# Performance work log

Hardware: AMD Instinct MI355X
Metric: run time of the kernel (lower is better)

Reference implementation:

```python
import jax, jax.numpy as jnp
import numpy as np

T, HID, H, KV, D = 2048, 2048, 16, 8, 128
EPS = 1e-6
THETA = 10000.0


def setup_inputs() -> dict:
    key = jax.random.key(0)
    ks = jax.random.split(key, 4)
    return {
        "positions": jnp.arange(T, dtype=jnp.int32),
        "hidden_states": jax.random.normal(ks[0], (T, HID), dtype=jnp.float32),
        "layernorm_weight": jnp.ones((HID,), dtype=jnp.float32),
        "qkv_weight": jax.random.normal(ks[1], ((H + 2 * KV) * D, HID), dtype=jnp.float32) * 0.02,
        "q_norm_weight": jnp.ones((D,), dtype=jnp.float32),
        "k_norm_weight": jnp.ones((D,), dtype=jnp.float32),
        "o_weight": jax.random.normal(ks[2], (HID, H * D), dtype=jnp.float32) * 0.02,
    }


def _rms(x, w, eps=EPS):
    var = jnp.mean(jnp.square(x), axis=-1, keepdims=True)
    return x * jax.lax.rsqrt(var + eps) * w


def _rope(x, pos):
    # NeoX-style rotary over full head_dim. x: [T, nH, D]
    inv_freq = 1.0 / (THETA ** (jnp.arange(0, D, 2, dtype=jnp.float32) / D))
    ang = pos.astype(jnp.float32)[:, None] * inv_freq  # [T, D/2]
    cos, sin = jnp.cos(ang)[:, None, :], jnp.sin(ang)[:, None, :]
    x1, x2 = x[..., : D // 2], x[..., D // 2 :]
    return jnp.concatenate([x1 * cos - x2 * sin, x2 * cos + x1 * sin], axis=-1)


def reference(positions, hidden_states, layernorm_weight, qkv_weight,
              q_norm_weight, k_norm_weight, o_weight):
    # Fused RMSNorm + QKV projection
    normed = _rms(hidden_states, layernorm_weight)                 # [T, HID]
    qkv = normed @ qkv_weight.T                                    # [T, (H+2KV)*D]
    q, k, v = jnp.split(qkv, [H * D, (H + KV) * D], axis=-1)
    q = _rms(q.reshape(T, H, D), q_norm_weight)                    # per-head q norm
    k = _rms(k.reshape(T, KV, D), k_norm_weight)                   # per-head k norm
    v = v.reshape(T, KV, D)
    # RoPE
    q = _rope(q, positions)
    k = _rope(k, positions)
    # GQA causal attention
    scale = D ** -0.5
    kr = jnp.repeat(k, H // KV, axis=1)                            # [T, H, D]
    vr = jnp.repeat(v, H // KV, axis=1)
    scores = jnp.einsum("qhd,khd->hqk", q, kr) * scale             # [H, T, T]
    mask = jnp.tril(jnp.ones((T, T), dtype=bool))
    scores = jnp.where(mask[None], scores, jnp.finfo(scores.dtype).min)
    attn = jax.nn.softmax(scores, axis=-1)
    out = jnp.einsum("hqk,khd->qhd", attn, vr).reshape(T, H * D)
    return out @ o_weight.T                                        # [T, HID]
```

## Files before the change

kernel.cpp:

```cpp
#include <hip/hip_runtime.h>
#include <cstdint>
#include <cstddef>

typedef __bf16 bf16;
typedef __attribute__((ext_vector_type(8))) __bf16 bf16x8;
typedef __attribute__((ext_vector_type(4))) __bf16 bf16x4v;
typedef __attribute__((ext_vector_type(4))) float f32x4;
typedef __attribute__((ext_vector_type(4))) short short4v;

#define T_N   2048
#define HID_N 2048
#define NH    16
#define NKV   8
#define HD    128

#define MFMA(a, b, c) __builtin_amdgcn_mfma_f32_16x16x32_bf16((a), (b), (c), 0, 0, 0)

__device__ __forceinline__ f32x4 MFMA16(short4v a, short4v b, f32x4 c) {
#if __has_builtin(__builtin_amdgcn_mfma_f32_16x16x16bf16_1k)
    return __builtin_amdgcn_mfma_f32_16x16x16bf16_1k(a, b, c, 0, 0, 0);
#else
    asm volatile("v_mfma_f32_16x16x16_bf16 %0, %1, %2, %0\n\ts_nop 7\n\ts_nop 7"
                 : "+v"(c) : "v"(a), "v"(b));
    return c;
#endif
}

__device__ __forceinline__ void gl_lds16(const void* g, void* l) {
    __builtin_amdgcn_global_load_lds(
        (const __attribute__((address_space(1))) unsigned int*)g,
        (__attribute__((address_space(3))) unsigned int*)l,
        16, 0, 0);
}

__device__ __forceinline__ uint32_t pk2(float a, float b) {
    union { bf16 h; unsigned short u; } ca, cb;
    ca.h = (bf16)a; cb.h = (bf16)b;
    return ((uint32_t)cb.u << 16) | ca.u;
}

__global__ __launch_bounds__(256) void k_f2b(const float* __restrict__ in,
                                             bf16* __restrict__ out, int n) {
    int i = (blockIdx.x * 256 + threadIdx.x) * 8;
    if (i >= n) return;
    const float4* p = (const float4*)(in + i);
    float4 a = p[0], b = p[1];
    bf16x8 v;
    v[0] = (bf16)a.x; v[1] = (bf16)a.y; v[2] = (bf16)a.z; v[3] = (bf16)a.w;
    v[4] = (bf16)b.x; v[5] = (bf16)b.y; v[6] = (bf16)b.z; v[7] = (bf16)b.w;
    *(bf16x8*)(out + i) = v;
}

__global__ __launch_bounds__(256) void k_rmsnorm(const float* __restrict__ x,
                                                 const float* __restrict__ w,
                                                 bf16* __restrict__ out) {
    int row = blockIdx.x, tid = threadIdx.x;
    const float* xr = x + (size_t)row * HID_N;
    float4 a = ((const float4*)xr)[tid * 2];
    float4 b = ((const float4*)xr)[tid * 2 + 1];
    float ss = a.x*a.x + a.y*a.y + a.z*a.z + a.w*a.w
             + b.x*b.x + b.y*b.y + b.z*b.z + b.w*b.w;
    #pragma unroll
    for (int m = 32; m; m >>= 1) ss += __shfl_xor(ss, m);
    __shared__ float red[4];
    if ((tid & 63) == 0) red[tid >> 6] = ss;
    __syncthreads();
    float tot = red[0] + red[1] + red[2] + red[3];
    float rs = rsqrtf(tot * (1.0f / HID_N) + 1e-6f);
    const float4* wr = (const float4*)(w + tid * 8);
    float4 wa = wr[0], wb = wr[1];
    bf16x8 v;
    v[0] = (bf16)(a.x * rs * wa.x); v[1] = (bf16)(a.y * rs * wa.y);
    v[2] = (bf16)(a.z * rs * wa.z); v[3] = (bf16)(a.w * rs * wa.w);
    v[4] = (bf16)(b.x * rs * wb.x); v[5] = (bf16)(b.y * rs * wb.y);
    v[6] = (bf16)(b.z * rs * wb.z); v[7] = (bf16)(b.w * rs * wb.w);
    *(bf16x8*)(out + (size_t)row * HID_N + tid * 8) = v;
}

__global__ __launch_bounds__(256, 3) void k_gemm_bt(const bf16* __restrict__ A,
                                                    const bf16* __restrict__ B,
                                                    float* __restrict__ C,
                                                    int M, int N, int K) {
    __shared__ __attribute__((aligned(16))) bf16 As[128 * 64];
    __shared__ __attribute__((aligned(16))) bf16 Bs[128 * 64];
    const int tid = threadIdx.x;
    const int lane = tid & 63, wid = tid >> 6;
    const int wm = wid >> 1, wn = wid & 1;
    const int r = lane & 15, g = lane >> 4;
    const size_t bm = (size_t)blockIdx.y * 128, bn = (size_t)blockIdx.x * 128;

    f32x4 acc[4][4] = {};

    const int srow = tid >> 3;
    const int schk = tid & 7;

    for (int k0 = 0; k0 < K; k0 += 64) {
        __syncthreads();
        #pragma unroll
        for (int c = 0; c < 4; c++) {
            int row = c * 32 + srow;
            int ka = (schk ^ (row & 7)) << 3;
            gl_lds16(A + (bm + row) * (size_t)K + k0 + ka,
                     (char*)As + c * 4096 + tid * 16);
            gl_lds16(B + (bn + row) * (size_t)K + k0 + ka,
                     (char*)Bs + c * 4096 + tid * 16);
        }
        __syncthreads();
        #pragma unroll
        for (int kk = 0; kk < 2; kk++) {
            bf16x8 af[4], bfr[4];
            #pragma unroll
            for (int m = 0; m < 4; m++) {
                int row = wm * 64 + m * 16 + r;
                af[m] = *(const bf16x8*)(As + row * 64 + (((kk * 4 + g) ^ (row & 7)) << 3));
            }
            #pragma unroll
            for (int n = 0; n < 4; n++) {
                int row = wn * 64 + n * 16 + r;
                bfr[n] = *(const bf16x8*)(Bs + row * 64 + (((kk * 4 + g) ^ (row & 7)) << 3));
            }
            #pragma unroll
            for (int m = 0; m < 4; m++)
                #pragma unroll
                for (int n = 0; n < 4; n++)
                    acc[m][n] = MFMA(af[m], bfr[n], acc[m][n]);
        }
    }
    #pragma unroll
    for (int m = 0; m < 4; m++)
        #pragma unroll
        for (int n = 0; n < 4; n++)
            #pragma unroll
            for (int j = 0; j < 4; j++) {
                size_t row = bm + wm * 64 + m * 16 + g * 4 + j;
                size_t col = bn + wn * 64 + n * 16 + r;
                C[row * (size_t)N + col] = acc[m][n][j];
            }
}

__global__ __launch_bounds__(256, 3) void k_gemm_qkv(const bf16* __restrict__ A,
                                                     const bf16* __restrict__ B,
                                                     bf16* __restrict__ qkv3,
                                                     bf16* __restrict__ vb) {
    const int K = HID_N;
    __shared__ __attribute__((aligned(16))) bf16 As[128 * 64];
    __shared__ __attribute__((aligned(16))) bf16 Bs[128 * 64];
    const int tid = threadIdx.x;
    const int lane = tid & 63, wid = tid >> 6;
    const int wm = wid >> 1, wn = wid & 1;
    const int r = lane & 15, g = lane >> 4;
    const size_t bm = (size_t)blockIdx.y * 128, bn = (size_t)blockIdx.x * 128;

    f32x4 acc[4][4] = {};
    const int srow = tid >> 3;
    const int schk = tid & 7;

    for (int k0 = 0; k0 < K; k0 += 64) {
        __syncthreads();
        #pragma unroll
        for (int c = 0; c < 4; c++) {
            int row = c * 32 + srow;
            int ka = (schk ^ (row & 7)) << 3;
            gl_lds16(A + (bm + row) * (size_t)K + k0 + ka,
                     (char*)As + c * 4096 + tid * 16);
            gl_lds16(B + (bn + row) * (size_t)K + k0 + ka,
                     (char*)Bs + c * 4096 + tid * 16);
        }
        __syncthreads();
        #pragma unroll
        for (int kk = 0; kk < 2; kk++) {
            bf16x8 af[4], bfr[4];
            #pragma unroll
            for (int m = 0; m < 4; m++) {
                int row = wm * 64 + m * 16 + r;
                af[m] = *(const bf16x8*)(As + row * 64 + (((kk * 4 + g) ^ (row & 7)) << 3));
            }
            #pragma unroll
            for (int n = 0; n < 4; n++) {
                int row = wn * 64 + n * 16 + r;
                bfr[n] = *(const bf16x8*)(Bs + row * 64 + (((kk * 4 + g) ^ (row & 7)) << 3));
            }
            #pragma unroll
            for (int m = 0; m < 4; m++)
                #pragma unroll
                for (int n = 0; n < 4; n++)
                    acc[m][n] = MFMA(af[m], bfr[n], acc[m][n]);
        }
    }
    #pragma unroll
    for (int m = 0; m < 4; m++)
        #pragma unroll
        for (int n = 0; n < 4; n++)
            #pragma unroll
            for (int j = 0; j < 4; j++) {
                size_t row = bm + wm * 64 + m * 16 + g * 4 + j;
                size_t col = bn + wn * 64 + n * 16 + r;
                bf16 val = (bf16)acc[m][n][j];
                if (col < 3072) qkv3[row * 3072 + col] = val;
                else            vb[row * 1024 + (col - 3072)] = val;
            }
}

__global__ __launch_bounds__(256) void k_vt(const bf16* __restrict__ in,
                                            bf16* __restrict__ outp) {
    __shared__ bf16 tile[64][72];
    const int tb = blockIdx.x;
    const int db = blockIdx.y;
    const int tid = threadIdx.x;
    const int row = tid >> 2, cc = tid & 3;
    const bf16* src = in + (size_t)(tb * 64 + row) * 1024 + db * 64 + cc * 16;
    bf16x8 a = *(const bf16x8*)(src);
    bf16x8 b = *(const bf16x8*)(src + 8);
    #pragma unroll
    for (int i = 0; i < 8; i++) tile[row][cc * 16 + i] = a[i];
    #pragma unroll
    for (int i = 0; i < 8; i++) tile[row][cc * 16 + 8 + i] = b[i];
    __syncthreads();
    bf16* dst = outp + (size_t)(db * 64 + row) * 2048 + tb * 64 + cc * 16;
    bf16x8 o1, o2;
    #pragma unroll
    for (int i = 0; i < 8; i++) o1[i] = tile[cc * 16 + i][row];
    #pragma unroll
    for (int i = 0; i < 8; i++) o2[i] = tile[cc * 16 + 8 + i][row];
    *(bf16x8*)dst = o1;
    *(bf16x8*)(dst + 8) = o2;
}

__global__ __launch_bounds__(256) void k_normrope(const bf16* __restrict__ qkv3,
                                                  const float* __restrict__ qw,
                                                  const float* __restrict__ kw,
                                                  const int* __restrict__ pos,
                                                  bf16* __restrict__ q,
                                                  bf16* __restrict__ k) {
    const int t = blockIdx.x, tid = threadIdx.x;
    const int half = tid >> 7, d = tid & 127;
    const int slot = blockIdx.y * 2 + half;
    const bool isq = slot < 16;
    const int h = isq ? slot : slot - 16;
    float x = (float)qkv3[(size_t)t * 3072 + slot * 128 + d];
    float ss = x * x;
    #pragma unroll
    for (int m = 32; m; m >>= 1) ss += __shfl_xor(ss, m);
    __shared__ float red[4];
    __shared__ float sh[256];
    if ((tid & 63) == 0) red[tid >> 6] = ss;
    __syncthreads();
    float rs = rsqrtf((red[half * 2] + red[half * 2 + 1]) * (1.0f / HD) + 1e-6f);
    float nx = x * rs * (isq ? qw[d] : kw[d]);
    sh[tid] = nx;
    __syncthreads();
    float other = sh[tid ^ 64];
    int j = d & 63;
    float ang = (float)pos[t] * __powf(10000.f, -(float)j * (1.f / 64.f));
    float s, c;
    __sincosf(ang, &s, &c);
    float o = (d < 64) ? (nx * c - other * s) : (nx * c + other * s);
    bf16* dst = isq ? (q + ((size_t)t * NH + h) * HD + d)
                    : (k + ((size_t)t * NKV + h) * HD + d);
    *dst = (bf16)o;
}

__global__ __launch_bounds__(256, 3) void k_flash(const bf16* __restrict__ Q,
                                                  const bf16* __restrict__ K,
                                                  const bf16* __restrict__ VT,
                                                  bf16* __restrict__ On,
                                                  float* __restrict__ ml) {
    __shared__ __attribute__((aligned(16))) bf16 Ks2[2][64 * 128];
    __shared__ __attribute__((aligned(16))) bf16 Vt[128 * 64];

    const int tid = threadIdx.x, lane = tid & 63, w = tid >> 6;
    const int r = lane & 15, g = lane >> 4;
    const int h = blockIdx.x, y = blockIdx.y;
    int ci, qt;
    if (y < 32)      { ci = 0; qt = y; }
    else if (y < 56) { ci = 1; qt = y - 24; }
    else if (y < 72) { ci = 2; qt = y - 40; }
    else             { ci = 3; qt = y - 48; }
    const int c0 = ci * 8;
    const int ntl = min(qt + 1 - c0, 8);
    const int q0 = qt * 64;
    const int gh = h >> 1;
    const int q0w = q0 + w * 16;

    const int rowk = tid >> 4, posc = tid & 15;
    const int vrow = tid >> 3, vkb = tid & 7;
    const bf16* VTh = VT + (size_t)gh * 128 * 2048;

    bf16x8 qf[4];
    #pragma unroll
    for (int ks = 0; ks < 4; ks++)
        qf[ks] = *(const bf16x8*)(Q + ((size_t)(q0w + r) * NH + h) * HD + ks * 32 + g * 8);

    f32x4 acc[8] = {};
    float m_run = -1e30f, l_run = 0.f;
    const float scale = 0.08838834764831845f;

    {
        const int kv0 = c0 * 64;
        #pragma unroll
        for (int c = 0; c < 4; c++) {
            int row = c * 16 + rowk;
            int srcc = posc ^ (row & 7);
            gl_lds16(K + ((size_t)(kv0 + row) * NKV + gh) * HD + srcc * 8,
                     (char*)&Ks2[0][0] + c * 4096 + tid * 16);
        }
        asm volatile("s_waitcnt vmcnt(0)" ::: "memory");
        __builtin_amdgcn_s_barrier();
    }

    for (int t = 0; t < ntl; ++t) {
        const int b = t & 1;
        const int kv0 = (c0 + t) * 64;
        const bool pf = (t + 1 < ntl);
        #pragma unroll
        for (int it = 0; it < 4; it++) {
            int d = it * 32 + vrow;
            int srck = (vkb ^ (vrow & 7)) * 8;
            gl_lds16(VTh + (size_t)d * 2048 + kv0 + srck,
                     (char*)&Vt[0] + it * 4096 + tid * 16);
        }
        if (pf) {
            const int kv1 = kv0 + 64;
            #pragma unroll
            for (int c = 0; c < 4; c++) {
                int row = c * 16 + rowk;
                int srcc = posc ^ (row & 7);
                gl_lds16(K + ((size_t)(kv1 + row) * NKV + gh) * HD + srcc * 8,
                         (char*)&Ks2[0][0] + (b ^ 1) * 16384 + c * 4096 + tid * 16);
            }
        }
        const bool compute = (kv0 <= q0w + 15);
        union PB { uint32_t u[2]; short4v s; };
        PB pbu[4];
        if (compute) {
            const bf16* Kb = &Ks2[b][0];
            const bool fullt = (kv0 + 63 <= q0w);
            float sc[4][4];
            __builtin_amdgcn_s_setprio(1);
            #pragma unroll
            for (int t4 = 0; t4 < 4; t4++) {
                f32x4 S = {};
                #pragma unroll
                for (int ks = 0; ks < 4; ks++) {
                    int row = t4 * 16 + r;
                    bf16x8 kf = *(const bf16x8*)(Kb + row * 128 + (((4 * ks + g) ^ (row & 7)) * 8));
                    S = MFMA(kf, qf[ks], S);
                }
                if (fullt) {
                    #pragma unroll
                    for (int j = 0; j < 4; j++) sc[t4][j] = S[j] * scale;
                } else {
                    #pragma unroll
                    for (int j = 0; j < 4; j++) {
                        int kg = kv0 + t4 * 16 + 4 * g + j;
                        sc[t4][j] = (kg <= q0w + r) ? S[j] * scale : -1e30f;
                    }
                }
            }
            __builtin_amdgcn_s_setprio(0);
            float mx = sc[0][0];
            #pragma unroll
            for (int t4 = 0; t4 < 4; t4++)
                #pragma unroll
                for (int j = 0; j < 4; j++) mx = fmaxf(mx, sc[t4][j]);
            mx = fmaxf(mx, __shfl_xor(mx, 16));
            mx = fmaxf(mx, __shfl_xor(mx, 32));
            const bool nr = __all(mx <= m_run + 8.0f) != 0;
            float mn, alpha;
            if (nr) { mn = m_run; alpha = 1.0f; }
            else    { mn = fmaxf(m_run, mx); alpha = __expf(m_run - mn); m_run = mn; }
            float rsum = 0.f;
            #pragma unroll
            for (int t4 = 0; t4 < 4; t4++)
                #pragma unroll
                for (int j = 0; j < 4; j++) {
                    sc[t4][j] = __expf(sc[t4][j] - mn);
                    rsum += sc[t4][j];
                }
            rsum += __shfl_xor(rsum, 16);
            rsum += __shfl_xor(rsum, 32);
            l_run = l_run * alpha + rsum;
            if (!nr) {
                #pragma unroll
                for (int f = 0; f < 8; f++)
                    #pragma unroll
                    for (int j = 0; j < 4; j++) acc[f][j] *= alpha;
            }
            #pragma unroll
            for (int t4 = 0; t4 < 4; t4++) {
                pbu[t4].u[0] = pk2(sc[t4][0], sc[t4][1]);
                pbu[t4].u[1] = pk2(sc[t4][2], sc[t4][3]);
            }
        }
        if (pf) asm volatile("s_waitcnt vmcnt(4)" ::: "memory");
        else    asm volatile("s_waitcnt vmcnt(0)" ::: "memory");
        __builtin_amdgcn_s_barrier();
        if (compute) {
            const char* Vb = (const char*)&Vt[0];
            __builtin_amdgcn_s_setprio(1);
            #pragma unroll
            for (int f = 0; f < 8; f++) {
                #pragma unroll
                for (int t4 = 0; t4 < 4; t4++) {
                    short4v vf = *(const short4v*)(Vb + f * 2048 + r * 128 +
                                  (((2 * t4 + (g >> 1)) ^ (r & 7)) * 16) + (g & 1) * 8);
                    acc[f] = MFMA16(vf, pbu[t4].s, acc[f]);
                }
            }
            __builtin_amdgcn_s_setprio(0);
        }
        asm volatile("s_waitcnt vmcnt(0)" ::: "memory");
        __builtin_amdgcn_s_barrier();
    }
    const int lr = w * 16 + r;
    float inv_l = 1.0f / l_run;
    bf16* Ob = On + ((size_t)(h * 80 + y)) * 8192 + lr * 128;
    #pragma unroll
    for (int f = 0; f < 8; f++) {
        bf16x4v ov;
        #pragma unroll
        for (int j = 0; j < 4; j++) ov[j] = (bf16)(acc[f][j] * inv_l);
        *(bf16x4v*)(Ob + f * 16 + 4 * g) = ov;
    }
    if (g == 0) {
        float* mlp = ml + ((size_t)(h * 80 + y)) * 128;
        mlp[lr] = m_run;
        mlp[64 + lr] = l_run;
    }
}

__global__ __launch_bounds__(256) void k_comb(const bf16* __restrict__ On,
                                              const float* __restrict__ ml,
                                              bf16* __restrict__ ao) {
    const int h = blockIdx.x, qt = blockIdx.y;
    const int lr = threadIdx.x & 63, db = threadIdx.x >> 6;
    const int nc = 1 + (qt >= 8) + (qt >= 16) + (qt >= 24);
    const int ys[4] = {qt, qt + 24, qt + 40, qt + 48};
    float mi[4], li[4], wi[4];
    float mstar = -1e30f;
    for (int i = 0; i < 4; i++) {
        if (i < nc) {
            const float* p = ml + ((size_t)(h * 80 + ys[i])) * 128;
            mi[i] = p[lr]; li[i] = p[64 + lr];
            mstar = fmaxf(mstar, mi[i]);
        }
    }
    float wsum = 0.f;
    for (int i = 0; i < 4; i++) {
        if (i < nc) { wi[i] = li[i] * __expf(mi[i] - mstar); wsum += wi[i]; }
        else wi[i] = 0.f;
    }
    float inv = 1.f / wsum;
    for (int i = 0; i < 4; i++) wi[i] *= inv;
    const int q = qt * 64 + lr;
    #pragma unroll
    for (int dd = 0; dd < 4; dd++) {
        int d0 = db * 32 + dd * 8;
        float o[8] = {};
        for (int i = 0; i < 4; i++) {
            if (i < nc) {
                bf16x8 v = *(const bf16x8*)(On + ((size_t)(h * 80 + ys[i])) * 8192 + lr * 128 + d0);
                #pragma unroll
                for (int j = 0; j < 8; j++) o[j] += wi[i] * (float)v[j];
            }
        }
        bf16x8 ov;
        #pragma unroll
        for (int j = 0; j < 8; j++) ov[j] = (bf16)o[j];
        *(bf16x8*)(ao + ((size_t)q * NH + h) * HD + d0) = ov;
    }
}

extern "C" void kernel_launch(void* const* d_in, const int* in_sizes, int n_in,
                              void* d_out, int out_size, void* d_ws, size_t ws_size,
                              hipStream_t stream) {
    const int*   pos  = (const int*)d_in[0];
    const float* hid  = (const float*)d_in[1];
    const float* lw   = (const float*)d_in[2];
    const float* qkvw = (const float*)d_in[3];
    const float* qnw  = (const float*)d_in[4];
    const float* knw  = (const float*)d_in[5];
    const float* ow   = (const float*)d_in[6];
    float* out = (float*)d_out;

    char* ws = (char*)d_ws;
    bf16*  qkvw_b = (bf16*)(ws);
    bf16*  ow_b   = (bf16*)(ws + (16u << 20));
    bf16*  normed = (bf16*)(ws + (24u << 20));
    bf16*  qkv3   = (bf16*)(ws + (32u << 20));
    bf16*  qb     = (bf16*)(ws + (64u << 20));
    bf16*  kb     = (bf16*)(ws + (72u << 20));
    bf16*  vb     = (bf16*)(ws + (76u << 20));
    bf16*  ao     = normed;
    bf16*  On     = (bf16*)(ws + (32u << 20));
    float* ml     = (float*)(ws + (54u << 20));
    bf16*  vT     = (bf16*)(ws + (56u << 20));

    k_f2b<<<4096, 256, 0, stream>>>(qkvw, qkvw_b, 4096 * 2048);
    k_f2b<<<2048, 256, 0, stream>>>(ow, ow_b, 2048 * 2048);
    k_rmsnorm<<<T_N, 256, 0, stream>>>(hid, lw, normed);
    k_gemm_qkv<<<dim3(32, 16), 256, 0, stream>>>(normed, qkvw_b, qkv3, vb);
    k_vt<<<dim3(32, 16), 256, 0, stream>>>(vb, vT);
    k_normrope<<<dim3(T_N, 12), 256, 0, stream>>>(qkv3, qnw, knw, pos, qb, kb);
    k_flash<<<dim3(NH, 80), 256, 0, stream>>>(qb, kb, vT, On, ml);
    k_comb<<<dim3(NH, 32), 256, 0, stream>>>(On, ml, ao);
    k_gemm_bt<<<dim3(16, 16), 256, 0, stream>>>(ao, ow_b, out, 2048, 2048, 2048);
}
```

Measured before the change: 182.4 us.

## Reorder flash split-KV block schedule heaviest-first and coalesce combine loads

Remaps the flash-attention grid's y index so that full 8-tile chunks are dispatched first, followed by partial chunks in decreasing size. This is a longest-job-first order meant to reduce tail imbalance across CUs. The combine kernel now uses a matching inverse mapping to find each chunk's partial results. Its thread layout changes so that 16 consecutive threads cover one row's 128 dims, which makes the On loads and ao stores contiguous. The cost is that each thread recomputes the softmax weights four times, once per row group.

```diff
diff --git a/kernel.cpp b/kernel.cpp
--- a/kernel.cpp
+++ b/kernel.cpp
@@ -37,6 +37,24 @@
     union { bf16 h; unsigned short u; } ca, cb;
     ca.h = (bf16)a; cb.h = (bf16)b;
     return ((uint32_t)cb.u << 16) | ca.u;
+}
+
+__device__ __forceinline__ void y2cq(int y, int& ci, int& qt) {
+    if (y < 25)       { ci = 0; qt = y + 7; }
+    else if (y < 42)  { ci = 1; qt = y - 10; }
+    else if (y < 51)  { ci = 2; qt = y - 19; }
+    else if (y == 51) { ci = 3; qt = 31; }
+    else { int z = y - 52; int k = 7 - (z >> 2); ci = z & 3; qt = 8 * ci + k - 1; }
+}
+__device__ __forceinline__ int yof(int ci, int qt) {
+    int k = qt + 1 - 8 * ci;
+    if (k >= 8) {
+        if (ci == 0) return qt - 7;
+        if (ci == 1) return qt + 10;
+        if (ci == 2) return qt + 19;
+        return 51;
+    }
+    return 52 + (7 - k) * 4 + ci;
 }
 
 __global__ __launch_bounds__(256) void k_f2b(const float* __restrict__ in,
@@ -272,10 +290,7 @@
     const int r = lane & 15, g = lane >> 4;
     const int h = blockIdx.x, y = blockIdx.y;
     int ci, qt;
-    if (y < 32)      { ci = 0; qt = y; }
-    else if (y < 56) { ci = 1; qt = y - 24; }
-    else if (y < 72) { ci = 2; qt = y - 40; }
-    else             { ci = 3; qt = y - 48; }
+    y2cq(y, ci, qt);
     const int c0 = ci * 8;
     const int ntl = min(qt + 1 - c0, 8);
     const int q0 = qt * 64;
@@ -433,41 +448,46 @@
                                               const float* __restrict__ ml,
                                               bf16* __restrict__ ao) {
     const int h = blockIdx.x, qt = blockIdx.y;
-    const int lr = threadIdx.x & 63, db = threadIdx.x >> 6;
+    const int tid = threadIdx.x;
+    const int dc = tid & 15;
+    const int qr = tid >> 4;
     const int nc = 1 + (qt >= 8) + (qt >= 16) + (qt >= 24);
-    const int ys[4] = {qt, qt + 24, qt + 40, qt + 48};
-    float mi[4], li[4], wi[4];
-    float mstar = -1e30f;
-    for (int i = 0; i < 4; i++) {
-        if (i < nc) {
-            const float* p = ml + ((size_t)(h * 80 + ys[i])) * 128;
-            mi[i] = p[lr]; li[i] = p[64 + lr];
-            mstar = fmaxf(mstar, mi[i]);
-        }
-    }
-    float wsum = 0.f;
-    for (int i = 0; i < 4; i++) {
-        if (i < nc) { wi[i] = li[i] * __expf(mi[i] - mstar); wsum += wi[i]; }
-        else wi[i] = 0.f;
-    }
-    float inv = 1.f / wsum;
-    for (int i = 0; i < 4; i++) wi[i] *= inv;
-    const int q = qt * 64 + lr;
-    #pragma unroll
-    for (int dd = 0; dd < 4; dd++) {
-        int d0 = db * 32 + dd * 8;
+    int ys[4];
+    #pragma unroll
+    for (int i = 0; i < 4; i++) ys[i] = (i < nc) ? yof(i, qt) : 0;
+    #pragma unroll
+    for (int p = 0; p < 4; p++) {
+        const int lq = p * 16 + qr;
+        float mi[4], li[4], wi[4];
+        float mstar = -1e30f;
+        for (int i = 0; i < 4; i++) {
+            if (i < nc) {
+                const float* pml = ml + ((size_t)(h * 80 + ys[i])) * 128;
+                mi[i] = pml[lq]; li[i] = pml[64 + lq];
+                mstar = fmaxf(mstar, mi[i]);
+            }
+        }
+        float wsum = 0.f;
+        for (int i = 0; i < 4; i++) {
+            if (i < nc) { wi[i] = li[i] * __expf(mi[i] - mstar); wsum += wi[i]; }
+            else wi[i] = 0.f;
+        }
+        float inv = 1.f / wsum;
         float o[8] = {};
         for (int i = 0; i < 4; i++) {
             if (i < nc) {
-                bf16x8 v = *(const bf16x8*)(On + ((size_t)(h * 80 + ys[i])) * 8192 + lr * 128 + d0);
-                #pragma unroll
-                for (int j = 0; j < 8; j++) o[j] += wi[i] * (float)v[j];
+                bf16x8 v = *(const bf16x8*)(On + ((size_t)(h * 80 + ys[i])) * 8192 +
+                                            lq * 128 + dc * 8);
+                float wn = wi[i] * inv;
+                #pragma unroll
+                for (int j = 0; j < 8; j++) o[j] += wn * (float)v[j];
             }
         }
         bf16x8 ov;
         #pragma unroll
         for (int j = 0; j < 8; j++) ov[j] = (bf16)o[j];
-        *(bf16x8*)(ao + ((size_t)q * NH + h) * HD + d0) = ov;
+        const int q = qt * 64 + lq;
+        *(bf16x8*)(ao + ((size_t)q * NH + h) * HD + dc * 8) = ov;
     }
 }
 
```

Result: no change. 181.9 us (-0.3%).
